# Kernel tuning notes

Measured on AMD Instinct MI355X. Metric: run time of the kernel, lower is better.

## Reference

```python
import jax, jax.numpy as jnp
import numpy as np

N_NODES = 50000
N_EDGES = 800000
IN_CH = 128
HIDDEN = 128
OUT_CH = 2
NUM_GRAPHS = 64


def setup_inputs() -> dict:
    key = jax.random.key(0)
    ks = jax.random.split(key, 12)
    x = jax.random.normal(ks[0], (N_NODES, IN_CH), dtype=jnp.float32)
    edge_index = jax.random.randint(ks[1], (2, N_EDGES), 0, N_NODES, dtype=jnp.int32)
    batch = jnp.sort(jax.random.randint(ks[2], (N_NODES,), 0, NUM_GRAPHS, dtype=jnp.int32))
    def glorot(k, fan_in, fan_out):
        s = (6.0 / (fan_in + fan_out)) ** 0.5
        return jax.random.uniform(k, (fan_in, fan_out), jnp.float32, -s, s)
    return {
        "x": x,
        "edge_index": edge_index,
        "batch": batch,
        "W1": glorot(ks[3], IN_CH, HIDDEN), "b1": jnp.zeros((HIDDEN,), jnp.float32),
        "W2": glorot(ks[4], HIDDEN, HIDDEN), "b2": jnp.zeros((HIDDEN,), jnp.float32),
        "W3": glorot(ks[5], HIDDEN, HIDDEN), "b3": jnp.zeros((HIDDEN,), jnp.float32),
        "Wc": glorot(ks[6], HIDDEN, OUT_CH), "bc": jnp.zeros((OUT_CH,), jnp.float32),
    }


def reference(x, edge_index, batch, W1, b1, W2, b2, W3, b3, Wc, bc):
    N = x.shape[0]
    src, dst = edge_index[0], edge_index[1]
    # GCN symmetric normalization with self-loops (PyG GCNConv default):
    # deg[i] = 1 (self loop) + in-degree
    deg = jax.ops.segment_sum(jnp.ones_like(src, jnp.float32), dst, num_segments=N) + 1.0
    dinv = deg ** -0.5                      # [N]
    edge_norm = (dinv[src] * dinv[dst])[:, None]   # [E,1]
    self_norm = (dinv * dinv)[:, None]             # [N,1]

    def gcn(h, W, b):
        hw = h @ W                                                    # [N,D]
        agg = jax.ops.segment_sum(edge_norm * hw[src], dst, num_segments=N)
        return agg + self_norm * hw + b

    h = jax.nn.relu(gcn(x, W1, b1))
    h = jax.nn.relu(gcn(h, W2, b2))
    h = jax.nn.relu(gcn(h, W3, b3))

    # global_mean_pool over batch ids
    counts = jax.ops.segment_sum(jnp.ones((N,), jnp.float32), batch, num_segments=NUM_GRAPHS)
    pooled = jax.ops.segment_sum(h, batch, num_segments=NUM_GRAPHS)
    pooled = pooled / jnp.maximum(counts, 1.0)[:, None]               # [G,D]

    return pooled @ Wc + bc                                           # [G,out]
```

## Files before the change

### kernel.cpp

```cpp
#include <hip/hip_runtime.h>

#define NCH 128
#define NGRAPH 64
#define SUB 16
#define CAP 64

typedef _Float16 h8 __attribute__((ext_vector_type(8)));
typedef float f32x4 __attribute__((ext_vector_type(4)));
typedef float f32x2 __attribute__((ext_vector_type(2)));


__device__ __forceinline__ unsigned pkh(float a, float b) {
    union { _Float16 h[2]; unsigned u; } x;
    x.h[0] = (_Float16)a; x.h[1] = (_Float16)b;
    return x.u;
}
__device__ __forceinline__ float flo(unsigned u) {
    union { unsigned u; _Float16 h[2]; } x; x.u = u; return (float)x.h[0];
}
__device__ __forceinline__ float fhi(unsigned u) {
    union { unsigned u; _Float16 h[2]; } x; x.u = u; return (float)x.h[1];
}
__device__ __forceinline__ unsigned short h16(float a) {
    union { _Float16 h; unsigned short s; } x; x.h = (_Float16)a; return x.s;
}

__device__ __forceinline__ float dinv_of(int cur, int n) {
    return rsqrtf((float)(cur - n * CAP) + 1.0f);
}


__global__ __launch_bounds__(256) void k_setup(const float* __restrict__ W1,
                                               const float* __restrict__ W2,
                                               const float* __restrict__ W3,
                                               uint4* __restrict__ wfrag,
                                               const int* __restrict__ batch,
                                               int* __restrict__ gstart,
                                               int* __restrict__ cursor, int N, int gN) {
    if (blockIdx.x < 24) {
        int gid = blockIdx.x * 256 + threadIdx.x;
        int layer = gid >> 11;
        int fr = gid & 2047;
        int c = fr >> 9;
        int nt = (fr >> 6) & 7;
        int i = fr & 63;
        int nl = i >> 2, q = i & 3;
        int iS = i ^ ((nl >> 1) & 7);
        int n = nt * 16 + nl;
        int k0 = c * 32 + q * 8;
        const float* W = (layer == 0) ? W1 : (layer == 1) ? W2 : W3;
        union { unsigned short s[8]; uint4 u; } pk;
        #pragma unroll
        for (int j = 0; j < 8; j++)
            pk.s[j] = h16(W[(k0 + j) * NCH + n]);
        wfrag[layer * 2048 + (c * 8 + nt) * 64 + iS] = pk.u;
    } else if (blockIdx.x < 24 + gN) {
        int i = (blockIdx.x - 24) * 256 + threadIdx.x;
        if (i >= N) return;
        int b = batch[i];
        int prev = (i == 0) ? -1 : batch[i - 1];
        for (int g = prev + 1; g <= b; g++) gstart[g] = i;
        if (i == N - 1) {
            for (int g = b + 1; g <= NGRAPH; g++) gstart[g] = N;
        }
    } else {
        int i = (blockIdx.x - 24 - gN) * 256 + threadIdx.x;
        if (i < N) cursor[i] = i * CAP;
    }
}

__global__ __launch_bounds__(256) void k_fill(const int* __restrict__ src,
                                              const int* __restrict__ dst,
                                              int* __restrict__ cursor,
                                              int* __restrict__ edge_src, int E, int N) {
    int range = blockIdx.x & 7;
    int chunk = blockIdx.x >> 3;
    int r0 = (range * N) >> 3;
    int r1 = ((range + 1) * N) >> 3;
    int e = chunk * 256 + threadIdx.x;
    if (e >= E) return;
    int d = dst[e];
    if (d >= r0 && d < r1) {
        int p = atomicAdd(&cursor[d], 1);
        if (p < (d + 1) * CAP) edge_src[p] = src[e];
    }
}


__global__ __launch_bounds__(256) void k_mmgemm(const void* __restrict__ Araw,
                                                const uint4* __restrict__ wfrag,
                                                const int* __restrict__ cursor,
                                                unsigned* __restrict__ D, int N,
                                                int a_fp32) {
    __shared__ uint4 Wl[2048];
    int t = threadIdx.x;
    #pragma unroll
    for (int i = 0; i < 8; i++) Wl[i * 256 + t] = wfrag[i * 256 + t];

    int wv = t >> 6, lane = t & 63;
    int rowW = blockIdx.x * 64 + wv * 16;
    int m = lane & 15, q = lane >> 4;
    int aRow = rowW + m;

    union { uint4 u; h8 h; } a[4];
    if (a_fp32) {
        const float* Af = (const float*)Araw;
        #pragma unroll
        for (int c = 0; c < 4; c++) {
            union { _Float16 h[8]; uint4 u; } pk;
            #pragma unroll
            for (int j = 0; j < 8; j++) pk.h[j] = (_Float16)0.f;
            if (aRow < N) {
                float4 v0 = *reinterpret_cast<const float4*>(&Af[(size_t)aRow * NCH + c * 32 + q * 8]);
                float4 v1 = *reinterpret_cast<const float4*>(&Af[(size_t)aRow * NCH + c * 32 + q * 8 + 4]);
                pk.h[0] = (_Float16)v0.x; pk.h[1] = (_Float16)v0.y;
                pk.h[2] = (_Float16)v0.z; pk.h[3] = (_Float16)v0.w;
                pk.h[4] = (_Float16)v1.x; pk.h[5] = (_Float16)v1.y;
                pk.h[6] = (_Float16)v1.z; pk.h[7] = (_Float16)v1.w;
            }
            a[c].u = pk.u;
        }
    } else {
        const unsigned* A = (const unsigned*)Araw;
        #pragma unroll
        for (int c = 0; c < 4; c++) {
            a[c].u = make_uint4(0, 0, 0, 0);
            if (aRow < N)
                a[c].u = *reinterpret_cast<const uint4*>(&A[(size_t)aRow * 64 + c * 16 + q * 4]);
        }
    }

    __syncthreads();

    int iS = (m * 4 + q) ^ ((m >> 1) & 7);

    f32x4 acc[8];
    #pragma unroll
    for (int nt = 0; nt < 8; nt++) acc[nt] = (f32x4){0.f, 0.f, 0.f, 0.f};

    #pragma unroll
    for (int c = 0; c < 4; c++) {
        #pragma unroll
        for (int nt = 0; nt < 8; nt++) {
            union { uint4 u; h8 h; } b;
            b.u = Wl[(c * 8 + nt) * 64 + iS];
            acc[nt] = __builtin_amdgcn_mfma_f32_16x16x32_f16(a[c].h, b.h, acc[nt], 0, 0, 0);
        }
    }

    float dn[4];
    #pragma unroll
    for (int r = 0; r < 4; r++) {
        int rg = rowW + q * 4 + r;
        dn[r] = (rg < N) ? dinv_of(cursor[rg], rg) : 0.0f;
    }
    #pragma unroll
    for (int nt = 0; nt < 8; nt++) {
        #pragma unroll
        for (int r = 0; r < 4; r++) {
            int rg = rowW + q * 4 + r;
            float v = acc[nt][r] * dn[r];
            unsigned b = __builtin_amdgcn_cvt_pk_fp8_f32(v, v, 0, false) & 0xffu;
            b |= ((unsigned)__shfl_xor((int)b, 1, 64)) << 8;
            b |= ((unsigned)__shfl_xor((int)b, 2, 64)) << 16;
            if ((lane & 3) == 0 && rg <= N)
                D[(size_t)rg * 32 + nt * 4 + (m >> 2)] = b;
        }
    }
}


__global__ __launch_bounds__(256) void k_gather(const unsigned short* __restrict__ hw,
                                                const float* __restrict__ bias,
                                                const int* __restrict__ cursor,
                                                const int* __restrict__ edge_src,
                                                unsigned* __restrict__ out, int N) {
    int wv = threadIdx.x >> 6;
    int lane = threadIdx.x & 63;
    int n = blockIdx.x * 4 + wv;
    if (n >= N) return;

    unsigned vs = hw[(size_t)n * 64 + lane];
    f32x2 v0 = __builtin_amdgcn_cvt_pk_f32_fp8((int)vs, false);
    float ax = v0.x, ay = v0.y;

    int j0 = n * CAP;
    int cur = cursor[n];
    int j1 = cur;
    if (j1 > j0 + CAP) j1 = j0 + CAP;

    int j = j0;
    for (; j + 16 <= j1; j += 16) {
        int myi = edge_src[j + (lane & 15)];
        unsigned u[16];
        #pragma unroll
        for (int i = 0; i < 16; i++) {
            int bi = __shfl(myi, i, 16);
            u[i] = hw[(size_t)bi * 64 + lane];
        }
        #pragma unroll
        for (int i = 0; i < 16; i++) {
            f32x2 v = __builtin_amdgcn_cvt_pk_f32_fp8((int)u[i], false);
            ax += v.x; ay += v.y;
        }
    }
    int r = j1 - j;
    if (r > 0) {
        int myi = edge_src[j + (lane & 15)];
        unsigned u[16];
        #pragma unroll
        for (int i = 0; i < 16; i++) {
            int bi = __shfl(myi, i, 16);
            bi = (i < r) ? bi : N;
            u[i] = hw[(size_t)bi * 64 + lane];
        }
        #pragma unroll
        for (int i = 0; i < 16; i++) {
            f32x2 v = __builtin_amdgcn_cvt_pk_f32_fp8((int)u[i], false);
            ax += v.x; ay += v.y;
        }
    }

    float dn = dinv_of(cur, n);
    float2 bb = reinterpret_cast<const float2*>(bias)[lane];
    float ox = fmaxf(ax * dn + bb.x, 0.0f);
    float oy = fmaxf(ay * dn + bb.y, 0.0f);
    out[(size_t)n * 64 + lane] = pkh(ox, oy);
}


__global__ __launch_bounds__(256) void k_poolA(const unsigned* __restrict__ h,
                                               const int* __restrict__ gstart,
                                               float* __restrict__ partial) {
    int g = blockIdx.x >> 4;
    int s = blockIdx.x & (SUB - 1);
    int c2 = threadIdx.x & 63;
    int r = threadIdx.x >> 6;
    int j0 = gstart[g], j1 = gstart[g + 1];
    int len = j1 - j0;
    int chunk = (len + SUB - 1) / SUB;
    int a0 = j0 + s * chunk;
    int a1 = a0 + chunk; if (a1 > j1) a1 = j1;
    float ax = 0.0f, ay = 0.0f;
    for (int j = a0 + r; j < a1; j += 4) {
        unsigned u = h[(size_t)j * 64 + c2];
        ax += flo(u); ay += fhi(u);
    }
    __shared__ float2 sh[4][64];
    sh[r][c2] = make_float2(ax, ay);
    __syncthreads();
    if (r == 0) {
        float sx = sh[0][c2].x + sh[1][c2].x + sh[2][c2].x + sh[3][c2].x;
        float sy = sh[0][c2].y + sh[1][c2].y + sh[2][c2].y + sh[3][c2].y;
        reinterpret_cast<float2*>(partial)[(size_t)(g * SUB + s) * 64 + c2] =
            make_float2(sx, sy);
    }
}

__global__ __launch_bounds__(128) void k_finalize(const float* __restrict__ partial,
                                                  const int* __restrict__ gstart,
                                                  const float* __restrict__ Wc,
                                                  const float* __restrict__ bc,
                                                  float* __restrict__ out) {
    int g = blockIdx.x;
    int c = threadIdx.x;
    float s = 0.0f;
    #pragma unroll
    for (int i = 0; i < SUB; i++) s += partial[(size_t)(g * SUB + i) * NCH + c];
    int len = gstart[g + 1] - gstart[g];
    __shared__ float sh[128];
    sh[c] = s / fmaxf((float)len, 1.0f);
    __syncthreads();
    if (c < 2) {
        float o = 0.0f;
        for (int k = 0; k < NCH; k++) o += sh[k] * Wc[k * 2 + c];
        out[g * 2 + c] = o + bc[c];
    }
}


extern "C" void kernel_launch(void* const* d_in, const int* in_sizes, int n_in,
                              void* d_out, int out_size, void* d_ws, size_t ws_size,
                              hipStream_t stream) {
    const float* x   = (const float*)d_in[0];
    const int* eidx  = (const int*)d_in[1];
    const int* batch = (const int*)d_in[2];
    const float* W1 = (const float*)d_in[3];
    const float* b1 = (const float*)d_in[4];
    const float* W2 = (const float*)d_in[5];
    const float* b2 = (const float*)d_in[6];
    const float* W3 = (const float*)d_in[7];
    const float* b3 = (const float*)d_in[8];
    const float* Wc = (const float*)d_in[9];
    const float* bc = (const float*)d_in[10];
    float* out = (float*)d_out;

    int N = in_sizes[0] / NCH;
    int E = in_sizes[1] / 2;
    const int* src = eidx;
    const int* dst = eidx + E;

    char* w = (char*)d_ws;
    auto alloc = [&](size_t bytes) -> void* {
        void* p = (void*)w;
        w += (bytes + 511) & ~(size_t)511;
        return p;
    };
    int*      cursor    = (int*)alloc((size_t)N * 4);
    int*      edge_src  = (int*)alloc((size_t)N * CAP * 4);
    uint4*    wfrag     = (uint4*)alloc((size_t)3 * 2048 * 16);
    unsigned* hwD       = (unsigned*)alloc((size_t)(N + 64) * 128);
    unsigned* hbA       = (unsigned*)alloc((size_t)N * 64 * 4);
    unsigned* hbB       = (unsigned*)alloc((size_t)N * 64 * 4);
    float*    partial   = (float*)alloc((size_t)NGRAPH * SUB * NCH * 4);
    int*      gstart    = (int*)alloc((size_t)(NGRAPH + 1) * 4);

    int gE = (E + 255) / 256;
    int gN = (N + 255) / 256;

    k_setup<<<24 + 2 * gN, 256, 0, stream>>>(W1, W2, W3, wfrag, batch, gstart, cursor, N, gN);
    k_fill<<<gE * 8, 256, 0, stream>>>(src, dst, cursor, edge_src, E, N);

    int gM = (N + 63) / 64;
    int gA = (N + 3) / 4;
    k_mmgemm<<<gM, 256, 0, stream>>>(x, wfrag, cursor, hwD, N, 1);
    k_gather<<<gA, 256, 0, stream>>>((const unsigned short*)hwD, b1, cursor, edge_src, hbA, N);
    k_mmgemm<<<gM, 256, 0, stream>>>(hbA, wfrag + 2048, cursor, hwD, N, 0);
    k_gather<<<gA, 256, 0, stream>>>((const unsigned short*)hwD, b2, cursor, edge_src, hbB, N);
    k_mmgemm<<<gM, 256, 0, stream>>>(hbB, wfrag + 4096, cursor, hwD, N, 0);
    k_gather<<<gA, 256, 0, stream>>>((const unsigned short*)hwD, b3, cursor, edge_src, hbA, N);

    k_poolA<<<NGRAPH * SUB, 256, 0, stream>>>(hbA, gstart, partial);
    k_finalize<<<NGRAPH, 128, 0, stream>>>(partial, gstart, Wc, bc, out);
}
```

Measured before the change: 247.3 us.

## Split fp8 hidden table into two channel halves for cache-resident gather

The GEMM now writes its fp8 output as two separate tables, each holding 64 channels per node, and the gather kernel runs twice as many blocks. Each block handles one half of the channels for 4 nodes, and interleaved block ordering keeps the two halves of neighboring nodes close in time. The aim is to halve the size of each gathered table so random neighbor reads hit L2/MALL cache more often. In exchange, each lane now does byte-sized loads and 16-bit stores, and the edge indices and cursor are read twice per node.

```diff
diff --git a/kernel.cpp b/kernel.cpp
--- a/kernel.cpp
+++ b/kernel.cpp
@@ -23,6 +23,10 @@
 }
 __device__ __forceinline__ unsigned short h16(float a) {
     union { _Float16 h; unsigned short s; } x; x.h = (_Float16)a; return x.s;
+}
+__device__ __forceinline__ float fp8lo(unsigned u) {
+    f32x2 v = __builtin_amdgcn_cvt_pk_f32_fp8((int)u, false);
+    return v.x;
 }
 
 __device__ __forceinline__ float dinv_of(int cur, int n) {
@@ -154,8 +158,10 @@
         int rg = rowW + q * 4 + r;
         dn[r] = (rg < N) ? dinv_of(cursor[rg], rg) : 0.0f;
     }
+    size_t tabDw = (size_t)(N + 64) * 16;
     #pragma unroll
     for (int nt = 0; nt < 8; nt++) {
+        unsigned* Dt = D + (nt >> 2) * tabDw;
         #pragma unroll
         for (int r = 0; r < 4; r++) {
             int rg = rowW + q * 4 + r;
@@ -164,25 +170,27 @@
             b |= ((unsigned)__shfl_xor((int)b, 1, 64)) << 8;
             b |= ((unsigned)__shfl_xor((int)b, 2, 64)) << 16;
             if ((lane & 3) == 0 && rg <= N)
-                D[(size_t)rg * 32 + nt * 4 + (m >> 2)] = b;
-        }
-    }
-}
-
-
-__global__ __launch_bounds__(256) void k_gather(const unsigned short* __restrict__ hw,
+                Dt[(size_t)rg * 16 + (nt & 3) * 4 + (m >> 2)] = b;
+        }
+    }
+}
+
+
+__global__ __launch_bounds__(256) void k_gather(const unsigned char* __restrict__ hw,
                                                 const float* __restrict__ bias,
                                                 const int* __restrict__ cursor,
                                                 const int* __restrict__ edge_src,
-                                                unsigned* __restrict__ out, int N) {
+                                                unsigned short* __restrict__ out, int N) {
+    int bb = blockIdx.x;
+    int h = (bb >> 2) & 1;
+    int ng = (bb >> 3) * 4 + (bb & 3);
     int wv = threadIdx.x >> 6;
     int lane = threadIdx.x & 63;
-    int n = blockIdx.x * 4 + wv;
+    int n = ng * 4 + wv;
     if (n >= N) return;
-
-    unsigned vs = hw[(size_t)n * 64 + lane];
-    f32x2 v0 = __builtin_amdgcn_cvt_pk_f32_fp8((int)vs, false);
-    float ax = v0.x, ay = v0.y;
+    const unsigned char* tab = hw + (size_t)h * (size_t)(N + 64) * 64;
+
+    float ax = fp8lo((unsigned)tab[(size_t)n * 64 + lane]);
 
     int j0 = n * CAP;
     int cur = cursor[n];
@@ -196,13 +204,11 @@
         #pragma unroll
         for (int i = 0; i < 16; i++) {
             int bi = __shfl(myi, i, 16);
-            u[i] = hw[(size_t)bi * 64 + lane];
-        }
-        #pragma unroll
-        for (int i = 0; i < 16; i++) {
-            f32x2 v = __builtin_amdgcn_cvt_pk_f32_fp8((int)u[i], false);
-            ax += v.x; ay += v.y;
-        }
+            u[i] = tab[(size_t)bi * 64 + lane];
+        }
+        #pragma unroll
+        for (int i = 0; i < 16; i++)
+            ax += fp8lo(u[i]);
     }
     int r = j1 - j;
     if (r > 0) {
@@ -212,20 +218,17 @@
         for (int i = 0; i < 16; i++) {
             int bi = __shfl(myi, i, 16);
             bi = (i < r) ? bi : N;
-            u[i] = hw[(size_t)bi * 64 + lane];
-        }
-        #pragma unroll
-        for (int i = 0; i < 16; i++) {
-            f32x2 v = __builtin_amdgcn_cvt_pk_f32_fp8((int)u[i], false);
-            ax += v.x; ay += v.y;
-        }
+            u[i] = tab[(size_t)bi * 64 + lane];
+        }
+        #pragma unroll
+        for (int i = 0; i < 16; i++)
+            ax += fp8lo(u[i]);
     }
 
     float dn = dinv_of(cur, n);
-    float2 bb = reinterpret_cast<const float2*>(bias)[lane];
-    float ox = fmaxf(ax * dn + bb.x, 0.0f);
-    float oy = fmaxf(ay * dn + bb.y, 0.0f);
-    out[(size_t)n * 64 + lane] = pkh(ox, oy);
+    float bb2 = bias[h * 64 + lane];
+    float ox = fmaxf(ax * dn + bb2, 0.0f);
+    out[(size_t)n * 128 + h * 64 + lane] = h16(ox);
 }
 
 
@@ -306,14 +309,14 @@
         w += (bytes + 511) & ~(size_t)511;
         return p;
     };
-    int*      cursor    = (int*)alloc((size_t)N * 4);
-    int*      edge_src  = (int*)alloc((size_t)N * CAP * 4);
-    uint4*    wfrag     = (uint4*)alloc((size_t)3 * 2048 * 16);
-    unsigned* hwD       = (unsigned*)alloc((size_t)(N + 64) * 128);
-    unsigned* hbA       = (unsigned*)alloc((size_t)N * 64 * 4);
-    unsigned* hbB       = (unsigned*)alloc((size_t)N * 64 * 4);
-    float*    partial   = (float*)alloc((size_t)NGRAPH * SUB * NCH * 4);
-    int*      gstart    = (int*)alloc((size_t)(NGRAPH + 1) * 4);
+    int*            cursor   = (int*)alloc((size_t)N * 4);
+    int*            edge_src = (int*)alloc((size_t)N * CAP * 4);
+    uint4*          wfrag    = (uint4*)alloc((size_t)3 * 2048 * 16);
+    unsigned*       hwD      = (unsigned*)alloc((size_t)2 * (N + 64) * 64);
+    unsigned short* hbA      = (unsigned short*)alloc((size_t)N * 256);
+    unsigned short* hbB      = (unsigned short*)alloc((size_t)N * 256);
+    float*          partial  = (float*)alloc((size_t)NGRAPH * SUB * NCH * 4);
+    int*            gstart   = (int*)alloc((size_t)(NGRAPH + 1) * 4);
 
     int gE = (E + 255) / 256;
     int gN = (N + 255) / 256;
@@ -322,14 +325,16 @@
     k_fill<<<gE * 8, 256, 0, stream>>>(src, dst, cursor, edge_src, E, N);
 
     int gM = (N + 63) / 64;
-    int gA = (N + 3) / 4;
+    int nb8 = (N + 15) / 16;
+    int gA = nb8 * 8;
+    const unsigned char* hw8 = (const unsigned char*)hwD;
     k_mmgemm<<<gM, 256, 0, stream>>>(x, wfrag, cursor, hwD, N, 1);
-    k_gather<<<gA, 256, 0, stream>>>((const unsigned short*)hwD, b1, cursor, edge_src, hbA, N);
+    k_gather<<<gA, 256, 0, stream>>>(hw8, b1, cursor, edge_src, hbA, N);
     k_mmgemm<<<gM, 256, 0, stream>>>(hbA, wfrag + 2048, cursor, hwD, N, 0);
-    k_gather<<<gA, 256, 0, stream>>>((const unsigned short*)hwD, b2, cursor, edge_src, hbB, N);
+    k_gather<<<gA, 256, 0, stream>>>(hw8, b2, cursor, edge_src, hbB, N);
     k_mmgemm<<<gM, 256, 0, stream>>>(hbB, wfrag + 4096, cursor, hwD, N, 0);
-    k_gather<<<gA, 256, 0, stream>>>((const unsigned short*)hwD, b3, cursor, edge_src, hbA, N);
-
-    k_poolA<<<NGRAPH * SUB, 256, 0, stream>>>(hbA, gstart, partial);
+    k_gather<<<gA, 256, 0, stream>>>(hw8, b3, cursor, edge_src, hbA, N);
+
+    k_poolA<<<NGRAPH * SUB, 256, 0, stream>>>((const unsigned*)hbA, gstart, partial);
     k_finalize<<<NGRAPH, 128, 0, stream>>>(partial, gstart, Wc, bc, out);
 }
```

Result: slower. 313.4 us (+26.7%).
